# Kernel tuning notes

Measured on AMD Instinct MI355X. Metric: run time of the kernel, lower is better.

Reference implementation:

```python
import jax, jax.numpy as jnp
from jax import lax
import numpy as np

T = 3          # boundary_kernel_size -> band width / dilation iterations
SDF_K = 3.0
ALPHA = 0.25   # focal alpha
GAMMA = 2.0    # focal gamma
TEMP = 1.5     # adaptive weighting temperature
SMOOTH = 1e-6  # iou smooth
EPS = 1e-12


def _maxpool3(x):
    # 3x3 max pool, stride 1, SAME padding on [B, H, W]
    return lax.reduce_window(x, -jnp.inf, lax.max, (1, 3, 3), (1, 1, 1), 'SAME')


def _bce_logits(x, t):
    # stable binary_cross_entropy_with_logits, elementwise
    return jnp.maximum(x, 0.0) - x * t + jnp.log1p(jnp.exp(-jnp.abs(x)))


def _limited_distance(mask, max_d):
    # iterative 3x3 dilation -> truncated distance-to-mask, values in {0..max_d, max_d+1}
    covered = mask > 0.5
    dist = jnp.where(covered, 0.0, float(max_d + 1)).astype(jnp.float32)
    for d in range(1, max_d + 1):
        covered_new = _maxpool3(covered.astype(jnp.float32)) > 0
        newly = jnp.logical_and(jnp.logical_not(covered), covered_new)
        dist = jnp.where(newly, float(d), dist)
        covered = covered_new
    return dist


def _boundary_loss(logits, target):
    p = jax.nn.sigmoid(logits)
    tb = (target > 0.5).astype(logits.dtype)
    outside_dist = _limited_distance(tb, T)        # distance to foreground
    inside_dist = _limited_distance(1.0 - tb, T)   # distance to background
    sdf = jnp.where(tb > 0.5, inside_dist, -outside_dist)
    band = (jnp.abs(sdf) <= float(T)).astype(logits.dtype)
    weight = (1.0 - jnp.abs(jnp.tanh(sdf / SDF_K))) * band
    pc = jnp.clip(p, EPS, 1.0 - EPS)
    bce = -(tb * jnp.log(pc) + (1.0 - tb) * jnp.log(1.0 - pc))
    denom = jnp.maximum(jnp.sum(weight, axis=(1, 2)), 1.0)
    return jnp.mean(jnp.sum(bce * weight, axis=(1, 2)) / denom)


def _focal_loss(logits, target):
    x = logits.reshape(logits.shape[0], -1)
    t = target.reshape(target.shape[0], -1)
    p = jax.nn.sigmoid(x)
    ce = _bce_logits(x, t)
    p_t = p * t + (1.0 - p) * (1.0 - t)
    loss = ce * (1.0 - p_t) ** GAMMA
    alpha_t = ALPHA * t + (1.0 - ALPHA) * (1.0 - t)
    loss = alpha_t * loss
    return jnp.mean(jnp.mean(loss, axis=1))


def _iou_loss(logits, target):
    p = jax.nn.sigmoid(logits).reshape(logits.shape[0], -1)
    t = target.reshape(target.shape[0], -1)
    inter = jnp.sum(p * t, axis=-1)
    union = jnp.sum(p, axis=-1) + jnp.sum(t, axis=-1) - inter
    iou = (inter + SMOOTH) / (union + SMOOTH)
    return jnp.mean(1.0 - iou)


def _dice_loss(logits, target):
    p = jax.nn.sigmoid(logits).reshape(logits.shape[0], -1)
    t = target.reshape(target.shape[0], -1)
    inter = jnp.sum(p * t, axis=-1)
    dice = (2.0 * inter + 1.0) / (jnp.sum(p, axis=-1) + jnp.sum(t, axis=-1) + 1.0)
    return jnp.mean(1.0 - dice)


def setup_inputs() -> dict:
    key = jax.random.key(0)
    k1, k2 = jax.random.split(key)
    B, H, W = 32, 1024, 1024
    pred = jax.random.normal(k1, (B, H, W), dtype=jnp.float32) * 2.0
    targets = (jax.random.uniform(k2, (B, H, W)) > 0.7).astype(jnp.float32)
    log_vars = jnp.log(jnp.array([1.0, 1.0, 0.5, 0.3, 0.2], dtype=jnp.float32))
    return {'pred': pred, 'targets': targets, 'log_vars': log_vars}


def reference(pred, targets, log_vars):
    target = targets.astype(pred.dtype)
    # 5 component losses, each pre-scaled by loss_scaling_factors
    ce = jnp.mean(_bce_logits(pred, target))                      # * 1.0
    dice = _dice_loss(pred, target)                               # * 1.0
    focal = 0.5 * _focal_loss(pred, target)
    iou = 0.3 * _iou_loss(pred, target)
    bnd = 0.2 * _boundary_loss(pred, target)
    losses = jnp.stack([ce, dice, focal, iou, bnd])
    # adaptive weighting (eval mode): normalized sigmoid of log_vars / temperature
    raw = jax.nn.sigmoid(log_vars / TEMP)
    weights = raw / jnp.sum(raw) * raw.shape[0]
    total = jnp.sum(weights * losses)
    return total
```

## Files before the change

kernel.cpp:

```cpp
#include <hip/hip_runtime.h>
#include <stdint.h>

#define HW    1024
#define BATCH 32
#define TR    16
#define HR    (TR + 6)
#define WN    32
#define TILES (HW / TR)
#define NBLK  (BATCH * TILES)

#define W1 0.6784872f
#define W2 0.4172171f
#define W3 0.2384058f

typedef float v2f __attribute__((ext_vector_type(2)));

static __device__ __forceinline__ v2f pk_fma(v2f a, v2f b, v2f c) {
    return __builtin_elementwise_fma(a, b, c);
}

__global__ __launch_bounds__(256) void k_main(const float* __restrict__ pred,
                                              const float* __restrict__ targ,
                                              float* __restrict__ ws) {
    __shared__ uint32_t fg[HR][WN];
    __shared__ uint4 plane[TR][WN];
    __shared__ float red[4][8];

    const int bid  = blockIdx.x;
    const int blk  = (bid & 7) * (NBLK / 8) + (bid >> 3);
    const int b    = blk / TILES;
    const int tile = blk - b * TILES;
    const int r0   = tile * TR;
    const int tid  = threadIdx.x;
    const int lane = tid & 63;
    const int wid  = tid >> 6;

    const float4* p4 = (const float4*)(pred + (size_t)b * HW * HW + (size_t)r0 * HW);
    float4 xa = p4[tid];
    float4 xb = p4[256 + tid];

    const float* tbase = targ + (size_t)b * HW * HW;
    for (int task = wid; task < HR * 4; task += 4) {
        const int row = task >> 2;
        const int g   = task & 3;
        const int gr  = r0 - 3 + row;
        uint32_t v = 0u;
        if (gr >= 0 && gr < HW) {
            const float4 t4 = *(const float4*)(tbase + (size_t)gr * HW + (g << 8) + (lane << 2));
            const uint32_t u0 = __float_as_uint(t4.x), u1 = __float_as_uint(t4.y);
            const uint32_t u2 = __float_as_uint(t4.z), u3 = __float_as_uint(t4.w);
            const uint32_t n = ((u0 >> 23) & 1u) | ((u1 >> 22) & 2u)
                             | ((u2 >> 21) & 4u) | ((u3 >> 20) & 8u);
            v = n << ((lane & 7) << 2);
        }
        v |= __shfl_xor(v, 1);
        v |= __shfl_xor(v, 2);
        v |= __shfl_xor(v, 4);
        if ((lane & 7) == 0) fg[row][(g << 3) + (lane >> 3)] = v;
    }
    __syncthreads();

    uint32_t ct = 0, c1 = 0, c2 = 0, c3 = 0;
    for (int i = tid; i < TR * WN; i += 256) {
        const int row = i >> 5;
        const int wz  = i & 31;
        const int hr  = row + 3;
        uint32_t v1c = 0, v2c = 0, v3c = 0, v1p = 0, v2p = 0, v3p = 0, v1n = 0, v2n = 0, v3n = 0;
        uint32_t u1c = 0, u2c = 0, u3c = 0, u1p = 0, u2p = 0, u3p = 0, u1n = 0, u2n = 0, u3n = 0;
        uint32_t tw = 0;
#pragma unroll
        for (int dr = -3; dr <= 3; ++dr) {
            const int r  = hr + dr;
            const int gr = r0 - 3 + r;
            const bool valid = (gr >= 0) && (gr < HW);
            const uint32_t c = fg[r][wz];
            const uint32_t p = (wz > 0)  ? fg[r][wz - 1] : 0u;
            const uint32_t n = (wz < 31) ? fg[r][wz + 1] : 0u;
            const uint32_t cb = valid ? ~c : 0u;
            const uint32_t pb = (valid && wz > 0)  ? ~p : 0u;
            const uint32_t nb = (valid && wz < 31) ? ~n : 0u;
            if (dr == 0) tw = c;
            v3c |= c;  v3p |= p;  v3n |= n;
            u3c |= cb; u3p |= pb; u3n |= nb;
            if (dr >= -2 && dr <= 2) {
                v2c |= c;  v2p |= p;  v2n |= n;
                u2c |= cb; u2p |= pb; u2n |= nb;
            }
            if (dr >= -1 && dr <= 1) {
                v1c |= c;  v1p |= p;  v1n |= n;
                u1c |= cb; u1p |= pb; u1n |= nb;
            }
        }
        const uint32_t d1f = v1c | (v1c << 1) | (v1p >> 31) | (v1c >> 1) | (v1n << 31);
        const uint32_t d2f = v2c | (v2c << 1) | (v2p >> 31) | (v2c >> 1) | (v2n << 31)
                                 | (v2c << 2) | (v2p >> 30) | (v2c >> 2) | (v2n << 30);
        const uint32_t d3f = v3c | (v3c << 1) | (v3p >> 31) | (v3c >> 1) | (v3n << 31)
                                 | (v3c << 2) | (v3p >> 30) | (v3c >> 2) | (v3n << 30)
                                 | (v3c << 3) | (v3p >> 29) | (v3c >> 3) | (v3n << 29);
        const uint32_t d1b = u1c | (u1c << 1) | (u1p >> 31) | (u1c >> 1) | (u1n << 31);
        const uint32_t d2b = u2c | (u2c << 1) | (u2p >> 31) | (u2c >> 1) | (u2n << 31)
                                 | (u2c << 2) | (u2p >> 30) | (u2c >> 2) | (u2n << 30);
        const uint32_t d3b = u3c | (u3c << 1) | (u3p >> 31) | (u3c >> 1) | (u3n << 31)
                                 | (u3c << 2) | (u3p >> 30) | (u3c >> 2) | (u3n << 30)
                                 | (u3c << 3) | (u3p >> 29) | (u3c >> 3) | (u3n << 29);
        uint4 pl;
        pl.x = tw;
        pl.y = (tw & d1b) | (~tw & d1f);
        pl.z = (tw & d2b) | (~tw & d2f);
        pl.w = (tw & d3b) | (~tw & d3f);
        plane[row][wz] = pl;
        ct += __popc(pl.x);
        c1 += __popc(pl.y);
        c2 += __popc(pl.z);
        c3 += __popc(pl.w);
    }
    __syncthreads();

    v2f a_pt = {0.f, 0.f}, a_p = {0.f, 0.f}, a_bw = {0.f, 0.f},
        a_ce = {0.f, 0.f}, a_f = {0.f, 0.f};
    const int wz = tid >> 3;
    const int sh = (tid & 7) << 2;

    const v2f dW12 = {W1 - W2, W1 - W2};
    const v2f dW23 = {W2 - W3, W2 - W3};
    const v2f cW3  = {W3, W3};
    const v2f kM2  = {-2.f, -2.f};
    const v2f kP1  = {1.f, 1.f};
    const v2f kMH  = {-0.5f, -0.5f};
    const v2f k34  = {0.75f, 0.75f};

    for (int rr = 0; rr < TR; ++rr) {
        const float4 cur = xa;
        xa = xb;
        if (rr + 2 < TR) xb = p4[(rr + 2) * 256 + tid];
        const uint4 pl = plane[rr][wz];
#pragma unroll
        for (int h = 0; h < 2; ++h) {
            v2f x;
            x.x = (h == 0) ? cur.x : cur.z;
            x.y = (h == 0) ? cur.y : cur.w;
            const int q0 = sh + (h << 1);

            v2f tf = {(float)((pl.x >> q0) & 1u), (float)((pl.x >> (q0 + 1)) & 1u)};
            v2f f1 = {(float)((pl.y >> q0) & 1u), (float)((pl.y >> (q0 + 1)) & 1u)};
            v2f f2 = {(float)((pl.z >> q0) & 1u), (float)((pl.z >> (q0 + 1)) & 1u)};
            v2f f3 = {(float)((pl.w >> q0) & 1u), (float)((pl.w >> (q0 + 1)) & 1u)};

            v2f ea;
            ea.x = fabsf(x.x) * -1.4426950408889634f;
            ea.y = fabsf(x.y) * -1.4426950408889634f;
            v2f e   = {__builtin_amdgcn_exp2f(ea.x), __builtin_amdgcn_exp2f(ea.y)};
            v2f opl = e + 1.0f;
            v2f inv = {__builtin_amdgcn_rcpf(opl.x), __builtin_amdgcn_rcpf(opl.y)};
            v2f lg  = {__builtin_amdgcn_logf(opl.x), __builtin_amdgcn_logf(opl.y)};
            v2f l1p = lg * 0.6931471805599453f;
            v2f pm  = 1.0f - inv;
            v2f p;
            p.x = (x.x >= 0.f) ? inv.x : pm.x;
            p.y = (x.y >= 0.f) ? inv.y : pm.y;

            v2f mx;
            mx.x = fmaxf(x.x, 0.f);
            mx.y = fmaxf(x.y, 0.f);
            v2f ce  = pk_fma(x, -tf, mx + l1p);

            v2f m2p = pk_fma(p, kM2, kP1);
            v2f omp = pk_fma(tf, m2p, p);
            v2f at  = pk_fma(tf, kMH, k34);
            v2f o2  = omp * omp;
            a_f  = pk_fma(o2 * at, ce, a_f);

            v2f w = pk_fma(f1, dW12, pk_fma(f2, dW23, f3 * cW3));
            a_bw = pk_fma(w, ce, a_bw);
            a_ce += ce;
            a_p  += p;
            a_pt  = pk_fma(tf, p, a_pt);
        }
    }

    float v[7];
    v[0] = a_pt.x + a_pt.y;
    v[1] = a_p.x + a_p.y;
    v[2] = (float)ct;
    v[3] = fmaf((float)c1, W1 - W2,
           fmaf((float)c2, W2 - W3, (float)c3 * W3));
    v[4] = a_bw.x + a_bw.y;
    v[5] = a_ce.x + a_ce.y;
    v[6] = a_f.x + a_f.y;
#pragma unroll
    for (int off = 1; off < 64; off <<= 1) {
#pragma unroll
        for (int j = 0; j < 7; ++j) v[j] += __shfl_xor(v[j], off);
    }
    if (lane == 0) {
#pragma unroll
        for (int j = 0; j < 7; ++j) red[wid][j] = v[j];
    }
    __syncthreads();
    if (tid < 7) {
        float s = red[0][tid] + red[1][tid] + red[2][tid] + red[3][tid];
        ws[tid * NBLK + blk] = s;
    }
}

__global__ __launch_bounds__(256) void k_tail(const float* __restrict__ ws,
                                              const float* __restrict__ lv,
                                              float* __restrict__ out) {
    __shared__ float res[7][BATCH];
    const int tid = threadIdx.x;
    const int b   = tid >> 3;
    const int g   = tid & 7;
#pragma unroll
    for (int q = 0; q < 7; ++q) {
        float s = 0.f;
#pragma unroll
        for (int i = 0; i < TILES / 8; ++i) s += ws[q * NBLK + b * TILES + g + i * 8];
        s += __shfl_xor(s, 1);
        s += __shfl_xor(s, 2);
        s += __shfl_xor(s, 4);
        if (g == 0) res[q][b] = s;
    }
    __syncthreads();
    if (tid < 32) {
        const float pt = res[0][tid];
        const float p  = res[1][tid];
        const float t  = res[2][tid];
        const float w  = res[3][tid];
        const float bw = res[4][tid];
        float d  = 1.f - (2.f * pt + 1.f) / (p + t + 1.f);
        float io = 1.f - (pt + 1e-6f) / (p + t - pt + 1e-6f);
        float bn = bw / fmaxf(w, 1.f);
        float ce = res[5][tid];
        float fo = res[6][tid];
#pragma unroll
        for (int off = 1; off < 32; off <<= 1) {
            d  += __shfl_xor(d, off);
            io += __shfl_xor(io, off);
            bn += __shfl_xor(bn, off);
            ce += __shfl_xor(ce, off);
            fo += __shfl_xor(fo, off);
        }
        if (tid == 0) {
            const float N = 33554432.f;
            float ls[5];
            ls[0] = ce / N;
            ls[1] = d * (1.f / 32.f);
            ls[2] = 0.5f * fo / N;
            ls[3] = 0.3f * io * (1.f / 32.f);
            ls[4] = 0.2f * bn * (1.f / 32.f);
            float r[5], s = 0.f;
#pragma unroll
            for (int i = 0; i < 5; ++i) {
                r[i] = 1.f / (1.f + __expf(-lv[i] * (1.f / 1.5f)));
                s += r[i];
            }
            float tot = 0.f;
#pragma unroll
            for (int i = 0; i < 5; ++i) tot += (r[i] / s) * 5.f * ls[i];
            out[0] = tot;
        }
    }
}

extern "C" void kernel_launch(void* const* d_in, const int* in_sizes, int n_in,
                              void* d_out, int out_size, void* d_ws, size_t ws_size,
                              hipStream_t stream) {
    const float* pred = (const float*)d_in[0];
    const float* targ = (const float*)d_in[1];
    const float* lv   = (const float*)d_in[2];
    float* out = (float*)d_out;
    float* ws  = (float*)d_ws;

    k_main<<<NBLK, 256, 0, stream>>>(pred, targ, ws);
    k_tail<<<1, 256, 0, stream>>>(ws, lv, out);
}
```

Before: 76.13 us.

## Double tile height, use 512-thread blocks, overlap halo target loads with plane build

Tile height goes from 16 to 32 rows and blocks grow to 512 threads, which cuts the relative cost of the 6-row target halo per tile. Target staging is split in two. The first 30 halo rows are packed first; the last rows are loaded into registers while the first half of the boundary plane is built, then packed. A mid-loop barrier lets the first half of the pixel loop start before the second half of the plane is visible. In exchange, register pressure and barrier count go up, and there are half as many blocks to spread across CUs.

```diff
diff --git a/kernel.cpp b/kernel.cpp
--- a/kernel.cpp
+++ b/kernel.cpp
@@ -3,11 +3,12 @@
 
 #define HW    1024
 #define BATCH 32
-#define TR    16
+#define TR    32
 #define HR    (TR + 6)
 #define WN    32
 #define TILES (HW / TR)
 #define NBLK  (BATCH * TILES)
+#define A1R   30
 
 #define W1 0.6784872f
 #define W2 0.4172171f
@@ -19,17 +20,127 @@
     return __builtin_elementwise_fma(a, b, c);
 }
 
-__global__ __launch_bounds__(256) void k_main(const float* __restrict__ pred,
-                                              const float* __restrict__ targ,
-                                              float* __restrict__ ws) {
+struct Acc { v2f pt, p, bw, ce, f; };
+
+static __device__ __forceinline__ void pix4(const float4 cur, const uint4 pl,
+                                            const int sh, Acc &a) {
+    const v2f dW12 = {W1 - W2, W1 - W2};
+    const v2f dW23 = {W2 - W3, W2 - W3};
+    const v2f cW3  = {W3, W3};
+    const v2f kM2  = {-2.f, -2.f};
+    const v2f kP1  = {1.f, 1.f};
+    const v2f kMH  = {-0.5f, -0.5f};
+    const v2f k34  = {0.75f, 0.75f};
+#pragma unroll
+    for (int h = 0; h < 2; ++h) {
+        v2f x;
+        x.x = (h == 0) ? cur.x : cur.z;
+        x.y = (h == 0) ? cur.y : cur.w;
+        const int q0 = sh + (h << 1);
+
+        v2f tf = {(float)((pl.x >> q0) & 1u), (float)((pl.x >> (q0 + 1)) & 1u)};
+        v2f f1 = {(float)((pl.y >> q0) & 1u), (float)((pl.y >> (q0 + 1)) & 1u)};
+        v2f f2 = {(float)((pl.z >> q0) & 1u), (float)((pl.z >> (q0 + 1)) & 1u)};
+        v2f f3 = {(float)((pl.w >> q0) & 1u), (float)((pl.w >> (q0 + 1)) & 1u)};
+
+        v2f ea;
+        ea.x = fabsf(x.x) * -1.4426950408889634f;
+        ea.y = fabsf(x.y) * -1.4426950408889634f;
+        v2f e   = {__builtin_amdgcn_exp2f(ea.x), __builtin_amdgcn_exp2f(ea.y)};
+        v2f opl = e + 1.0f;
+        v2f inv = {__builtin_amdgcn_rcpf(opl.x), __builtin_amdgcn_rcpf(opl.y)};
+        v2f lg  = {__builtin_amdgcn_logf(opl.x), __builtin_amdgcn_logf(opl.y)};
+        v2f l1p = lg * 0.6931471805599453f;
+        v2f pm  = 1.0f - inv;
+        v2f p;
+        p.x = (x.x >= 0.f) ? inv.x : pm.x;
+        p.y = (x.y >= 0.f) ? inv.y : pm.y;
+
+        v2f mx;
+        mx.x = fmaxf(x.x, 0.f);
+        mx.y = fmaxf(x.y, 0.f);
+        v2f ce  = pk_fma(x, -tf, mx + l1p);
+
+        v2f m2p = pk_fma(p, kM2, kP1);
+        v2f omp = pk_fma(tf, m2p, p);
+        v2f at  = pk_fma(tf, kMH, k34);
+        v2f o2  = omp * omp;
+        a.f  = pk_fma(o2 * at, ce, a.f);
+
+        v2f w = pk_fma(f1, dW12, pk_fma(f2, dW23, f3 * cW3));
+        a.bw = pk_fma(w, ce, a.bw);
+        a.ce += ce;
+        a.p  += p;
+        a.pt  = pk_fma(tf, p, a.pt);
+    }
+}
+
+static __device__ __forceinline__ void build_plane(
+    const uint32_t (*fg)[WN], uint4 (*plane)[WN], int row, int wz, int r0,
+    uint32_t &ct, uint32_t &c1, uint32_t &c2, uint32_t &c3)
+{
+    const int hr = row + 3;
+    uint32_t v1c = 0, v2c = 0, v3c = 0, v1p = 0, v2p = 0, v3p = 0, v1n = 0, v2n = 0, v3n = 0;
+    uint32_t u1c = 0, u2c = 0, u3c = 0, u1p = 0, u2p = 0, u3p = 0, u1n = 0, u2n = 0, u3n = 0;
+    uint32_t tw = 0;
+#pragma unroll
+    for (int dr = -3; dr <= 3; ++dr) {
+        const int r  = hr + dr;
+        const int gr = r0 - 3 + r;
+        const bool valid = (gr >= 0) && (gr < HW);
+        const uint32_t c = fg[r][wz];
+        const uint32_t p = (wz > 0)  ? fg[r][wz - 1] : 0u;
+        const uint32_t n = (wz < 31) ? fg[r][wz + 1] : 0u;
+        const uint32_t cb = valid ? ~c : 0u;
+        const uint32_t pb = (valid && wz > 0)  ? ~p : 0u;
+        const uint32_t nb = (valid && wz < 31) ? ~n : 0u;
+        if (dr == 0) tw = c;
+        v3c |= c;  v3p |= p;  v3n |= n;
+        u3c |= cb; u3p |= pb; u3n |= nb;
+        if (dr >= -2 && dr <= 2) {
+            v2c |= c;  v2p |= p;  v2n |= n;
+            u2c |= cb; u2p |= pb; u2n |= nb;
+        }
+        if (dr >= -1 && dr <= 1) {
+            v1c |= c;  v1p |= p;  v1n |= n;
+            u1c |= cb; u1p |= pb; u1n |= nb;
+        }
+    }
+    const uint32_t d1f = v1c | (v1c << 1) | (v1p >> 31) | (v1c >> 1) | (v1n << 31);
+    const uint32_t d2f = v2c | (v2c << 1) | (v2p >> 31) | (v2c >> 1) | (v2n << 31)
+                             | (v2c << 2) | (v2p >> 30) | (v2c >> 2) | (v2n << 30);
+    const uint32_t d3f = v3c | (v3c << 1) | (v3p >> 31) | (v3c >> 1) | (v3n << 31)
+                             | (v3c << 2) | (v3p >> 30) | (v3c >> 2) | (v3n << 30)
+                             | (v3c << 3) | (v3p >> 29) | (v3c >> 3) | (v3n << 29);
+    const uint32_t d1b = u1c | (u1c << 1) | (u1p >> 31) | (u1c >> 1) | (u1n << 31);
+    const uint32_t d2b = u2c | (u2c << 1) | (u2p >> 31) | (u2c >> 1) | (u2n << 31)
+                             | (u2c << 2) | (u2p >> 30) | (u2c >> 2) | (u2n << 30);
+    const uint32_t d3b = u3c | (u3c << 1) | (u3p >> 31) | (u3c >> 1) | (u3n << 31)
+                             | (u3c << 2) | (u3p >> 30) | (u3c >> 2) | (u3n << 30)
+                             | (u3c << 3) | (u3p >> 29) | (u3c >> 3) | (u3n << 29);
+    uint4 pl;
+    pl.x = tw;
+    pl.y = (tw & d1b) | (~tw & d1f);
+    pl.z = (tw & d2b) | (~tw & d2f);
+    pl.w = (tw & d3b) | (~tw & d3f);
+    plane[row][wz] = pl;
+    ct += __popc(pl.x);
+    c1 += __popc(pl.y);
+    c2 += __popc(pl.z);
+    c3 += __popc(pl.w);
+}
+
+__global__ __launch_bounds__(512, 8) void k_main(const float* __restrict__ pred,
+                                                 const float* __restrict__ targ,
+                                                 float* __restrict__ ws) {
     __shared__ uint32_t fg[HR][WN];
     __shared__ uint4 plane[TR][WN];
-    __shared__ float red[4][8];
+    __shared__ float red[8][8];
 
     const int bid  = blockIdx.x;
     const int blk  = (bid & 7) * (NBLK / 8) + (bid >> 3);
-    const int b    = blk / TILES;
-    const int tile = blk - b * TILES;
+    const int b    = blk >> 5;
+    const int tile = blk & 31;
     const int r0   = tile * TR;
     const int tid  = threadIdx.x;
     const int lane = tid & 63;
@@ -37,10 +148,12 @@
 
     const float4* p4 = (const float4*)(pred + (size_t)b * HW * HW + (size_t)r0 * HW);
     float4 xa = p4[tid];
-    float4 xb = p4[256 + tid];
+    float4 xb = p4[tid + 512];
 
     const float* tbase = targ + (size_t)b * HW * HW;
-    for (int task = wid; task < HR * 4; task += 4) {
+#pragma unroll
+    for (int it = 0; it < (A1R * 4) / 8; ++it) {
+        const int task = wid + it * 8;
         const int row = task >> 2;
         const int g   = task & 3;
         const int gr  = r0 - 3 + row;
@@ -60,133 +173,77 @@
     }
     __syncthreads();
 
+    float4 t4s[4];
+    bool   vl2[4];
+#pragma unroll
+    for (int it = 0; it < 4; ++it) {
+        const int task = A1R * 4 + wid + it * 8;
+        const int row = task >> 2;
+        const int g   = task & 3;
+        const int gr  = r0 - 3 + row;
+        vl2[it] = (gr >= 0) && (gr < HW);
+        if (vl2[it])
+            t4s[it] = *(const float4*)(tbase + (size_t)gr * HW + (g << 8) + (lane << 2));
+    }
+
     uint32_t ct = 0, c1 = 0, c2 = 0, c3 = 0;
-    for (int i = tid; i < TR * WN; i += 256) {
-        const int row = i >> 5;
-        const int wz  = i & 31;
-        const int hr  = row + 3;
-        uint32_t v1c = 0, v2c = 0, v3c = 0, v1p = 0, v2p = 0, v3p = 0, v1n = 0, v2n = 0, v3n = 0;
-        uint32_t u1c = 0, u2c = 0, u3c = 0, u1p = 0, u2p = 0, u3p = 0, u1n = 0, u2n = 0, u3n = 0;
-        uint32_t tw = 0;
-#pragma unroll
-        for (int dr = -3; dr <= 3; ++dr) {
-            const int r  = hr + dr;
-            const int gr = r0 - 3 + r;
-            const bool valid = (gr >= 0) && (gr < HW);
-            const uint32_t c = fg[r][wz];
-            const uint32_t p = (wz > 0)  ? fg[r][wz - 1] : 0u;
-            const uint32_t n = (wz < 31) ? fg[r][wz + 1] : 0u;
-            const uint32_t cb = valid ? ~c : 0u;
-            const uint32_t pb = (valid && wz > 0)  ? ~p : 0u;
-            const uint32_t nb = (valid && wz < 31) ? ~n : 0u;
-            if (dr == 0) tw = c;
-            v3c |= c;  v3p |= p;  v3n |= n;
-            u3c |= cb; u3p |= pb; u3n |= nb;
-            if (dr >= -2 && dr <= 2) {
-                v2c |= c;  v2p |= p;  v2n |= n;
-                u2c |= cb; u2p |= pb; u2n |= nb;
-            }
-            if (dr >= -1 && dr <= 1) {
-                v1c |= c;  v1p |= p;  v1n |= n;
-                u1c |= cb; u1p |= pb; u1n |= nb;
-            }
-        }
-        const uint32_t d1f = v1c | (v1c << 1) | (v1p >> 31) | (v1c >> 1) | (v1n << 31);
-        const uint32_t d2f = v2c | (v2c << 1) | (v2p >> 31) | (v2c >> 1) | (v2n << 31)
-                                 | (v2c << 2) | (v2p >> 30) | (v2c >> 2) | (v2n << 30);
-        const uint32_t d3f = v3c | (v3c << 1) | (v3p >> 31) | (v3c >> 1) | (v3n << 31)
-                                 | (v3c << 2) | (v3p >> 30) | (v3c >> 2) | (v3n << 30)
-                                 | (v3c << 3) | (v3p >> 29) | (v3c >> 3) | (v3n << 29);
-        const uint32_t d1b = u1c | (u1c << 1) | (u1p >> 31) | (u1c >> 1) | (u1n << 31);
-        const uint32_t d2b = u2c | (u2c << 1) | (u2p >> 31) | (u2c >> 1) | (u2n << 31)
-                                 | (u2c << 2) | (u2p >> 30) | (u2c >> 2) | (u2n << 30);
-        const uint32_t d3b = u3c | (u3c << 1) | (u3p >> 31) | (u3c >> 1) | (u3n << 31)
-                                 | (u3c << 2) | (u3p >> 30) | (u3c >> 2) | (u3n << 30)
-                                 | (u3c << 3) | (u3p >> 29) | (u3c >> 3) | (u3n << 29);
-        uint4 pl;
-        pl.x = tw;
-        pl.y = (tw & d1b) | (~tw & d1f);
-        pl.z = (tw & d2b) | (~tw & d2f);
-        pl.w = (tw & d3b) | (~tw & d3f);
-        plane[row][wz] = pl;
-        ct += __popc(pl.x);
-        c1 += __popc(pl.y);
-        c2 += __popc(pl.z);
-        c3 += __popc(pl.w);
-    }
-    __syncthreads();
-
-    v2f a_pt = {0.f, 0.f}, a_p = {0.f, 0.f}, a_bw = {0.f, 0.f},
-        a_ce = {0.f, 0.f}, a_f = {0.f, 0.f};
-    const int wz = tid >> 3;
-    const int sh = (tid & 7) << 2;
-
-    const v2f dW12 = {W1 - W2, W1 - W2};
-    const v2f dW23 = {W2 - W3, W2 - W3};
-    const v2f cW3  = {W3, W3};
-    const v2f kM2  = {-2.f, -2.f};
-    const v2f kP1  = {1.f, 1.f};
-    const v2f kMH  = {-0.5f, -0.5f};
-    const v2f k34  = {0.75f, 0.75f};
-
-    for (int rr = 0; rr < TR; ++rr) {
+    build_plane(fg, plane, tid >> 5, tid & 31, r0, ct, c1, c2, c3);
+
+#pragma unroll
+    for (int it = 0; it < 4; ++it) {
+        const int task = A1R * 4 + wid + it * 8;
+        const int row = task >> 2;
+        const int g   = task & 3;
+        uint32_t v = 0u;
+        if (vl2[it]) {
+            const uint32_t u0 = __float_as_uint(t4s[it].x), u1 = __float_as_uint(t4s[it].y);
+            const uint32_t u2 = __float_as_uint(t4s[it].z), u3 = __float_as_uint(t4s[it].w);
+            const uint32_t n = ((u0 >> 23) & 1u) | ((u1 >> 22) & 2u)
+                             | ((u2 >> 21) & 4u) | ((u3 >> 20) & 8u);
+            v = n << ((lane & 7) << 2);
+        }
+        v |= __shfl_xor(v, 1);
+        v |= __shfl_xor(v, 2);
+        v |= __shfl_xor(v, 4);
+        if ((lane & 7) == 0) fg[row][(g << 3) + (lane >> 3)] = v;
+    }
+    __syncthreads();
+
+    build_plane(fg, plane, 16 + (tid >> 5), tid & 31, r0, ct, c1, c2, c3);
+
+    Acc a;
+    a.pt = (v2f){0.f, 0.f}; a.p = (v2f){0.f, 0.f}; a.bw = (v2f){0.f, 0.f};
+    a.ce = (v2f){0.f, 0.f}; a.f = (v2f){0.f, 0.f};
+    const int wzc = (tid & 255) >> 3;
+    const int sh  = (tid & 7) << 2;
+    const int rofs = tid >> 8;
+
+    int kk = 0;
+    for (; kk < 8; ++kk) {
         const float4 cur = xa;
         xa = xb;
-        if (rr + 2 < TR) xb = p4[(rr + 2) * 256 + tid];
-        const uint4 pl = plane[rr][wz];
-#pragma unroll
-        for (int h = 0; h < 2; ++h) {
-            v2f x;
-            x.x = (h == 0) ? cur.x : cur.z;
-            x.y = (h == 0) ? cur.y : cur.w;
-            const int q0 = sh + (h << 1);
-
-            v2f tf = {(float)((pl.x >> q0) & 1u), (float)((pl.x >> (q0 + 1)) & 1u)};
-            v2f f1 = {(float)((pl.y >> q0) & 1u), (float)((pl.y >> (q0 + 1)) & 1u)};
-            v2f f2 = {(float)((pl.z >> q0) & 1u), (float)((pl.z >> (q0 + 1)) & 1u)};
-            v2f f3 = {(float)((pl.w >> q0) & 1u), (float)((pl.w >> (q0 + 1)) & 1u)};
-
-            v2f ea;
-            ea.x = fabsf(x.x) * -1.4426950408889634f;
-            ea.y = fabsf(x.y) * -1.4426950408889634f;
-            v2f e   = {__builtin_amdgcn_exp2f(ea.x), __builtin_amdgcn_exp2f(ea.y)};
-            v2f opl = e + 1.0f;
-            v2f inv = {__builtin_amdgcn_rcpf(opl.x), __builtin_amdgcn_rcpf(opl.y)};
-            v2f lg  = {__builtin_amdgcn_logf(opl.x), __builtin_amdgcn_logf(opl.y)};
-            v2f l1p = lg * 0.6931471805599453f;
-            v2f pm  = 1.0f - inv;
-            v2f p;
-            p.x = (x.x >= 0.f) ? inv.x : pm.x;
-            p.y = (x.y >= 0.f) ? inv.y : pm.y;
-
-            v2f mx;
-            mx.x = fmaxf(x.x, 0.f);
-            mx.y = fmaxf(x.y, 0.f);
-            v2f ce  = pk_fma(x, -tf, mx + l1p);
-
-            v2f m2p = pk_fma(p, kM2, kP1);
-            v2f omp = pk_fma(tf, m2p, p);
-            v2f at  = pk_fma(tf, kMH, k34);
-            v2f o2  = omp * omp;
-            a_f  = pk_fma(o2 * at, ce, a_f);
-
-            v2f w = pk_fma(f1, dW12, pk_fma(f2, dW23, f3 * cW3));
-            a_bw = pk_fma(w, ce, a_bw);
-            a_ce += ce;
-            a_p  += p;
-            a_pt  = pk_fma(tf, p, a_pt);
-        }
+        if (kk + 2 < 16) xb = p4[tid + (kk + 2) * 512];
+        const uint4 pl = plane[2 * kk + rofs][wzc];
+        pix4(cur, pl, sh, a);
+    }
+    __syncthreads();
+    for (; kk < 16; ++kk) {
+        const float4 cur = xa;
+        xa = xb;
+        if (kk + 2 < 16) xb = p4[tid + (kk + 2) * 512];
+        const uint4 pl = plane[2 * kk + rofs][wzc];
+        pix4(cur, pl, sh, a);
     }
 
     float v[7];
-    v[0] = a_pt.x + a_pt.y;
-    v[1] = a_p.x + a_p.y;
+    v[0] = a.pt.x + a.pt.y;
+    v[1] = a.p.x + a.p.y;
     v[2] = (float)ct;
     v[3] = fmaf((float)c1, W1 - W2,
            fmaf((float)c2, W2 - W3, (float)c3 * W3));
-    v[4] = a_bw.x + a_bw.y;
-    v[5] = a_ce.x + a_ce.y;
-    v[6] = a_f.x + a_f.y;
+    v[4] = a.bw.x + a.bw.y;
+    v[5] = a.ce.x + a.ce.y;
+    v[6] = a.f.x + a.f.y;
 #pragma unroll
     for (int off = 1; off < 64; off <<= 1) {
 #pragma unroll
@@ -198,7 +255,9 @@
     }
     __syncthreads();
     if (tid < 7) {
-        float s = red[0][tid] + red[1][tid] + red[2][tid] + red[3][tid];
+        float s = 0.f;
+#pragma unroll
+        for (int wv = 0; wv < 8; ++wv) s += red[wv][tid];
         ws[tid * NBLK + blk] = s;
     }
 }
@@ -271,6 +330,6 @@
     float* out = (float*)d_out;
     float* ws  = (float*)d_ws;
 
-    k_main<<<NBLK, 256, 0, stream>>>(pred, targ, ws);
+    k_main<<<NBLK, 512, 0, stream>>>(pred, targ, ws);
     k_tail<<<1, 256, 0, stream>>>(ws, lv, out);
 }
```

Result: slower. 90.51 us (+18.9%).

## Split fused kernel into target bit-plane pass and per-pixel loss pass

Applied to the files above, without the earlier changes.

Splits the single fused kernel in two. The first kernel builds the distance bit-planes from the targets and writes them to a global workspace along with their per-tile counts. The second kernel streams pred together with the precomputed bit-planes to accumulate the per-pixel losses. This is meant to lower per-kernel register and LDS pressure and to avoid serialising target decoding before the pred math. The cost is an extra launch and a global write and read of the bit-planes, about 16 MB.

```diff
diff --git a/kernel.cpp b/kernel.cpp
--- a/kernel.cpp
+++ b/kernel.cpp
@@ -19,12 +19,11 @@
     return __builtin_elementwise_fma(a, b, c);
 }
 
-__global__ __launch_bounds__(256) void k_main(const float* __restrict__ pred,
-                                              const float* __restrict__ targ,
+__global__ __launch_bounds__(256) void k_bits(const float* __restrict__ targ,
+                                              uint4* __restrict__ plane_g,
                                               float* __restrict__ ws) {
     __shared__ uint32_t fg[HR][WN];
-    __shared__ uint4 plane[TR][WN];
-    __shared__ float red[4][8];
+    __shared__ float red[4][2];
 
     const int bid  = blockIdx.x;
     const int blk  = (bid & 7) * (NBLK / 8) + (bid >> 3);
@@ -34,10 +33,6 @@
     const int tid  = threadIdx.x;
     const int lane = tid & 63;
     const int wid  = tid >> 6;
-
-    const float4* p4 = (const float4*)(pred + (size_t)b * HW * HW + (size_t)r0 * HW);
-    float4 xa = p4[tid];
-    float4 xb = p4[256 + tid];
 
     const float* tbase = targ + (size_t)b * HW * HW;
     for (int task = wid; task < HR * 4; task += 4) {
@@ -108,16 +103,44 @@
         pl.y = (tw & d1b) | (~tw & d1f);
         pl.z = (tw & d2b) | (~tw & d2f);
         pl.w = (tw & d3b) | (~tw & d3f);
-        plane[row][wz] = pl;
+        plane_g[((size_t)b * HW + r0 + row) * WN + wz] = pl;
         ct += __popc(pl.x);
         c1 += __popc(pl.y);
         c2 += __popc(pl.z);
         c3 += __popc(pl.w);
     }
+
+    float vt = (float)ct;
+    float vw = fmaf((float)c1, W1 - W2, fmaf((float)c2, W2 - W3, (float)c3 * W3));
+#pragma unroll
+    for (int off = 1; off < 64; off <<= 1) {
+        vt += __shfl_xor(vt, off);
+        vw += __shfl_xor(vw, off);
+    }
+    if (lane == 0) { red[wid][0] = vt; red[wid][1] = vw; }
     __syncthreads();
-
-    v2f a_pt = {0.f, 0.f}, a_p = {0.f, 0.f}, a_bw = {0.f, 0.f},
-        a_ce = {0.f, 0.f}, a_f = {0.f, 0.f};
+    if (tid < 2) {
+        float s = red[0][tid] + red[1][tid] + red[2][tid] + red[3][tid];
+        ws[(2 + tid) * NBLK + blk] = s;
+    }
+}
+
+__global__ __launch_bounds__(256) void k_pix(const float* __restrict__ pred,
+                                             const uint4* __restrict__ plane_g,
+                                             float* __restrict__ ws) {
+    __shared__ float red[4][5];
+
+    const int bid  = blockIdx.x;
+    const int blk  = (bid & 7) * (NBLK / 8) + (bid >> 3);
+    const int b    = blk / TILES;
+    const int tile = blk - b * TILES;
+    const int r0   = tile * TR;
+    const int tid  = threadIdx.x;
+    const int lane = tid & 63;
+    const int wid  = tid >> 6;
+
+    const float4* p4 = (const float4*)(pred + (size_t)b * HW * HW + (size_t)r0 * HW);
+    const uint4*  pg = plane_g + ((size_t)b * HW + r0) * WN;
     const int wz = tid >> 3;
     const int sh = (tid & 7) << 2;
 
@@ -129,11 +152,22 @@
     const v2f kMH  = {-0.5f, -0.5f};
     const v2f k34  = {0.75f, 0.75f};
 
+    v2f a_pt = {0.f, 0.f}, a_p = {0.f, 0.f}, a_bw = {0.f, 0.f},
+        a_ce = {0.f, 0.f}, a_f = {0.f, 0.f};
+
+    float4 xa = p4[tid];
+    float4 xb = p4[256 + tid];
+    uint4  qa = pg[wz];
+    uint4  qb = pg[WN + wz];
+
     for (int rr = 0; rr < TR; ++rr) {
         const float4 cur = xa;
-        xa = xb;
-        if (rr + 2 < TR) xb = p4[(rr + 2) * 256 + tid];
-        const uint4 pl = plane[rr][wz];
+        const uint4  pl  = qa;
+        xa = xb; qa = qb;
+        if (rr + 2 < TR) {
+            xb = p4[(rr + 2) * 256 + tid];
+            qb = pg[(rr + 2) * WN + wz];
+        }
 #pragma unroll
         for (int h = 0; h < 2; ++h) {
             v2f x;
@@ -178,28 +212,26 @@
         }
     }
 
-    float v[7];
+    float v[5];
     v[0] = a_pt.x + a_pt.y;
     v[1] = a_p.x + a_p.y;
-    v[2] = (float)ct;
-    v[3] = fmaf((float)c1, W1 - W2,
-           fmaf((float)c2, W2 - W3, (float)c3 * W3));
-    v[4] = a_bw.x + a_bw.y;
-    v[5] = a_ce.x + a_ce.y;
-    v[6] = a_f.x + a_f.y;
+    v[2] = a_bw.x + a_bw.y;
+    v[3] = a_ce.x + a_ce.y;
+    v[4] = a_f.x + a_f.y;
 #pragma unroll
     for (int off = 1; off < 64; off <<= 1) {
 #pragma unroll
-        for (int j = 0; j < 7; ++j) v[j] += __shfl_xor(v[j], off);
+        for (int j = 0; j < 5; ++j) v[j] += __shfl_xor(v[j], off);
     }
     if (lane == 0) {
 #pragma unroll
-        for (int j = 0; j < 7; ++j) red[wid][j] = v[j];
+        for (int j = 0; j < 5; ++j) red[wid][j] = v[j];
     }
     __syncthreads();
-    if (tid < 7) {
+    if (tid < 5) {
         float s = red[0][tid] + red[1][tid] + red[2][tid] + red[3][tid];
-        ws[tid * NBLK + blk] = s;
+        const int q = (tid == 0) ? 0 : (tid == 1) ? 1 : (tid == 2) ? 4 : (tid == 3) ? 5 : 6;
+        ws[q * NBLK + blk] = s;
     }
 }
 
@@ -270,7 +302,9 @@
     const float* lv   = (const float*)d_in[2];
     float* out = (float*)d_out;
     float* ws  = (float*)d_ws;
-
-    k_main<<<NBLK, 256, 0, stream>>>(pred, targ, ws);
+    uint4* plane_g = (uint4*)(ws + 7 * NBLK);
+
+    k_bits<<<NBLK, 256, 0, stream>>>(targ, plane_g, ws);
+    k_pix <<<NBLK, 256, 0, stream>>>(pred, plane_g, ws);
     k_tail<<<1, 256, 0, stream>>>(ws, lv, out);
 }
```

Measured after the change: 90.52 us. +18.9%, slower.

## Software-pipeline target bitmask loads and deepen pred prefetch to four rows

Applied to the files above, without the earlier changes.

The target bitmask build now has each thread load two float4s (8 floats) per task and pack them into a byte written directly to shared memory. This removes the wave shuffle reductions, and loads are issued two slots ahead of consumption to keep more memory requests in flight. The pred row prefetch is deepened from two rows to four, and the main row loop is fully unrolled so the register ring indices are static. These changes raise register pressure, and the byte-granular shared stores may cause bank conflicts.

```diff
diff --git a/kernel.cpp b/kernel.cpp
--- a/kernel.cpp
+++ b/kernel.cpp
@@ -8,6 +8,8 @@
 #define WN    32
 #define TILES (HW / TR)
 #define NBLK  (BATCH * TILES)
+#define NTASK (HR * 128)
+#define TPT   (NTASK / 256)
 
 #define W1 0.6784872f
 #define W2 0.4172171f
@@ -18,6 +20,48 @@
 static __device__ __forceinline__ v2f pk_fma(v2f a, v2f b, v2f c) {
     return __builtin_elementwise_fma(a, b, c);
 }
+
+#define A_ISSUE(slot, m)                                                        \
+    do {                                                                        \
+        _Pragma("unroll")                                                       \
+        for (int j = 0; j < 2; ++j) {                                           \
+            const int k = 2 * (m) + j;                                          \
+            if (k < TPT) {                                                      \
+                const int task = tid + (k << 8);                                \
+                const int gr   = r0 - 3 + (task >> 7);                          \
+                if (gr >= 0 && gr < HW) {                                       \
+                    const float4* rp = (const float4*)(tbase + (size_t)gr * HW);\
+                    sa[slot][j] = rp[(task & 127) * 2];                         \
+                    sb[slot][j] = rp[(task & 127) * 2 + 1];                     \
+                }                                                               \
+            }                                                                   \
+        }                                                                       \
+    } while (0)
+
+#define A_CONSUME(slot, m)                                                      \
+    do {                                                                        \
+        _Pragma("unroll")                                                       \
+        for (int j = 0; j < 2; ++j) {                                           \
+            const int k = 2 * (m) + j;                                          \
+            if (k < TPT) {                                                      \
+                const int task = tid + (k << 8);                                \
+                const int row  = task >> 7;                                     \
+                const int gr   = r0 - 3 + row;                                  \
+                uint32_t n = 0u;                                                \
+                if (gr >= 0 && gr < HW) {                                       \
+                    n  =  (__float_as_uint(sa[slot][j].x) >> 23) & 1u;          \
+                    n |= ((__float_as_uint(sa[slot][j].y) >> 23) & 1u) << 1;    \
+                    n |= ((__float_as_uint(sa[slot][j].z) >> 23) & 1u) << 2;    \
+                    n |= ((__float_as_uint(sa[slot][j].w) >> 23) & 1u) << 3;    \
+                    n |= ((__float_as_uint(sb[slot][j].x) >> 23) & 1u) << 4;    \
+                    n |= ((__float_as_uint(sb[slot][j].y) >> 23) & 1u) << 5;    \
+                    n |= ((__float_as_uint(sb[slot][j].z) >> 23) & 1u) << 6;    \
+                    n |= ((__float_as_uint(sb[slot][j].w) >> 23) & 1u) << 7;    \
+                }                                                               \
+                fg8[row * 128 + (task & 127)] = (uint8_t)n;                     \
+            }                                                                   \
+        }                                                                       \
+    } while (0)
 
 __global__ __launch_bounds__(256) void k_main(const float* __restrict__ pred,
                                               const float* __restrict__ targ,
@@ -36,28 +80,22 @@
     const int wid  = tid >> 6;
 
     const float4* p4 = (const float4*)(pred + (size_t)b * HW * HW + (size_t)r0 * HW);
-    float4 xa = p4[tid];
-    float4 xb = p4[256 + tid];
-
     const float* tbase = targ + (size_t)b * HW * HW;
-    for (int task = wid; task < HR * 4; task += 4) {
-        const int row = task >> 2;
-        const int g   = task & 3;
-        const int gr  = r0 - 3 + row;
-        uint32_t v = 0u;
-        if (gr >= 0 && gr < HW) {
-            const float4 t4 = *(const float4*)(tbase + (size_t)gr * HW + (g << 8) + (lane << 2));
-            const uint32_t u0 = __float_as_uint(t4.x), u1 = __float_as_uint(t4.y);
-            const uint32_t u2 = __float_as_uint(t4.z), u3 = __float_as_uint(t4.w);
-            const uint32_t n = ((u0 >> 23) & 1u) | ((u1 >> 22) & 2u)
-                             | ((u2 >> 21) & 4u) | ((u3 >> 20) & 8u);
-            v = n << ((lane & 7) << 2);
-        }
-        v |= __shfl_xor(v, 1);
-        v |= __shfl_xor(v, 2);
-        v |= __shfl_xor(v, 4);
-        if ((lane & 7) == 0) fg[row][(g << 3) + (lane >> 3)] = v;
-    }
+    uint8_t* fg8 = (uint8_t*)&fg[0][0];
+
+    float4 sa[2][2], sb[2][2];
+    A_ISSUE(0, 0);
+    A_ISSUE(1, 1);
+    A_CONSUME(0, 0);  A_ISSUE(0, 2);
+    A_CONSUME(1, 1);  A_ISSUE(1, 3);
+    A_CONSUME(0, 2);  A_ISSUE(0, 4);
+    A_CONSUME(1, 3);  A_ISSUE(1, 5);
+    A_CONSUME(0, 4);
+    A_CONSUME(1, 5);
+
+    float4 xq[4];
+#pragma unroll
+    for (int i = 0; i < 4; ++i) xq[i] = p4[i * 256 + tid];
     __syncthreads();
 
     uint32_t ct = 0, c1 = 0, c2 = 0, c3 = 0;
@@ -129,10 +167,10 @@
     const v2f kMH  = {-0.5f, -0.5f};
     const v2f k34  = {0.75f, 0.75f};
 
+#pragma unroll
     for (int rr = 0; rr < TR; ++rr) {
-        const float4 cur = xa;
-        xa = xb;
-        if (rr + 2 < TR) xb = p4[(rr + 2) * 256 + tid];
+        const float4 cur = xq[rr & 3];
+        if (rr + 4 < TR) xq[rr & 3] = p4[(rr + 4) * 256 + tid];
         const uint4 pl = plane[rr][wz];
 #pragma unroll
         for (int h = 0; h < 2; ++h) {
```

Result: slower. 90.43 us (+18.8%).
